# Performance work log

Measured on AMD Instinct MI355X. Metric: run time of the kernel, lower is better.

Reference implementation:

```python
import jax, jax.numpy as jnp
import numpy as np

BS, P, N, D, H = 2, 512, 2048, 768, 12
HD = D // H  # 64


def _lg_forward(input_xs, input_xq, xs_mask, qkv_w, qkv_b, proj_w, proj_b):
    bs, P_, D_ = input_xs.shape
    N_ = input_xq.shape[1]
    d = D_ // H
    scale = 1.0 / jnp.sqrt(jnp.asarray(d, input_xs.dtype))

    # concat order is [xq, xs] in the original
    xsq = jnp.concatenate([input_xq, input_xs], axis=1)          # [bs, N+P, D]
    full_qkv = xsq @ qkv_w + qkv_b                               # [bs, N+P, 3D]

    # faithful quirk: first P rows -> 'xs' qkv, remaining N rows -> 'xq' qkv
    xs_qkv = full_qkv[:, :P_].reshape(bs, P_, 3, H, d).transpose(2, 0, 3, 1, 4)
    xq_qkv = full_qkv[:, P_:].reshape(bs, N_, 3, H, d).transpose(2, 0, 3, 1, 4)
    xs_q, xs_k, xs_v = xs_qkv[0], xs_qkv[1], xs_qkv[2]           # [bs,H,P,d]
    xq_q, xq_k, xq_v = xq_qkv[0], xq_qkv[1], xq_qkv[2]           # [bs,H,N,d]

    # cross attention: xq queries attend over concat([xs, xq]) keys/values
    cross_k = jnp.concatenate([xs_k, xq_k], axis=2)              # [bs,H,P+N,d]
    cross_v = jnp.concatenate([xs_v, xq_v], axis=2)              # [bs,H,P+N,d]
    cross_scores = jnp.einsum('bhnd,bhmd->bhnm', xq_q, cross_k)  # [bs,H,N,P+N]
    cross_mask = jnp.pad(xs_mask, ((0, 0), (0, N_)))[:, None, None, :]
    cross_scores = jnp.where(cross_mask, -jnp.inf, cross_scores) * scale
    cross_probs = jax.nn.softmax(cross_scores, axis=-1)
    cross_out = jnp.einsum('bhnm,bhmd->bhnd', cross_probs, cross_v)
    cross_out = cross_out.transpose(0, 2, 1, 3).reshape(bs, N_, D_)  # [bs,N,D]

    # xs self attention
    self_scores = jnp.einsum('bhpd,bhqd->bhpq', xs_q, xs_k)      # [bs,H,P,P]
    self_scores = jnp.where(xs_mask[:, None, None, :], -jnp.inf, self_scores) * scale
    self_probs = jax.nn.softmax(self_scores, axis=-1)
    xs_out = jnp.einsum('bhpq,bhqd->bhpd', self_probs, xs_v)     # [bs,H,P,d]
    # faithful quirk: original does .transpose(-2,-1).view(bs,P,-1)
    xs_out = xs_out.transpose(0, 1, 3, 2).reshape(bs, P_, D_)    # [bs,P,D] (scrambled layout)

    out = jnp.concatenate([xs_out, cross_out], axis=1) @ proj_w + proj_b
    return out[:, :P_], out[:, P_:]


def setup_inputs() -> dict:
    key = jax.random.key(0)
    ks = jax.random.split(key, 6)
    return {
        'input_xs': jax.random.normal(ks[0], (BS, P, D), jnp.float32),
        'input_xq': jax.random.normal(ks[1], (BS, N, D), jnp.float32),
        'xs_mask': jax.random.randint(ks[2], (BS, P), 0, 2).astype(bool),
        'qkv_w': jax.random.normal(ks[3], (D, 3 * D), jnp.float32) * (D ** -0.5),
        'qkv_b': jnp.zeros((3 * D,), jnp.float32),
        'proj_w': jax.random.normal(ks[4], (D, D), jnp.float32) * (D ** -0.5),
        'proj_b': jnp.zeros((D,), jnp.float32),
    }


def reference(input_xs, input_xq, xs_mask, qkv_w, qkv_b, proj_w, proj_b):
    return _lg_forward(input_xs, input_xq, xs_mask, qkv_w, qkv_b, proj_w, proj_b)
```

## Files before the change

### kernel.cpp

```cpp
#include <hip/hip_runtime.h>
#include <hip/hip_bf16.h>

#define BS   2
#define PP   512
#define NN   2048
#define DD   768
#define HH   12
#define HD   64
#define RTOT 2560
#define QKVC 2304
#define MTOT (BS * RTOT)
#define CROWS (BS * HH * NN)
#define SROWS (BS * HH * PP)
#define TROWS (CROWS + SROWS)

typedef __attribute__((ext_vector_type(8))) short  short8;
typedef __attribute__((ext_vector_type(4))) float  floatx4;

#define MFMA16(a, b, c) __builtin_amdgcn_mfma_f32_16x16x32_bf16(a, b, c, 0, 0, 0)
#define LOG2E 1.4426950408889634f
#define SCL2  0.18033688011112042f

__device__ __forceinline__ float bf2f(unsigned short x) {
    union { unsigned u; float f; } c; c.u = ((unsigned)x) << 16; return c.f;
}
__device__ __forceinline__ unsigned short f2bf(float x) {
    union { float f; unsigned u; } c; c.f = x;
    unsigned r = c.u + 0x7fff + ((c.u >> 16) & 1);
    return (unsigned short)(r >> 16);
}

__device__ __forceinline__ float4 load4(const void* p, size_t i, bool f32) {
    if (f32) return *(const float4*)((const float*)p + i);
    ushort4 u = *(const ushort4*)((const unsigned short*)p + i);
    return make_float4(bf2f(u.x), bf2f(u.y), bf2f(u.z), bf2f(u.w));
}
__device__ __forceinline__ float load1(const void* p, size_t i, bool f32) {
    return f32 ? ((const float*)p)[i] : bf2f(((const unsigned short*)p)[i]);
}
__device__ __forceinline__ bool mask_at(const void* m, int idx, int mtype) {
    if (mtype == 2) return ((const float*)m)[idx] != 0.0f;
    if (mtype == 1) return ((const unsigned char*)m)[idx] != 0;
    return ((const int*)m)[idx] != 0;
}
__device__ __forceinline__ void store_out(float* p, size_t i, float v) { p[i] = v; }
__device__ __forceinline__ void store_out(__hip_bfloat16* p, size_t i, float v) {
    p[i] = __float2bfloat16(v);
}

__device__ __forceinline__ void gload_lds16(const unsigned short* g, unsigned short* l) {
    __builtin_amdgcn_global_load_lds(
        (const __attribute__((address_space(1))) void*)g,
        (__attribute__((address_space(3))) void*)l,
        16, 0, 0);
}

__device__ __forceinline__ int sigma_pos(int k) {
    return (k & 0x23) | ((k & 0x0C) << 1) | ((k & 0x10) >> 2);
}
__device__ __forceinline__ int sigma_inv(int p) {
    return (p & 0x23) | ((p & 0x18) >> 1) | ((p & 0x04) << 2);
}

__global__ void detect_kernel(const void* __restrict__ w,
                              const void* __restrict__ mask,
                              int* __restrict__ flags,
                              float* __restrict__ mb, int do_mb) {
    __shared__ int s_f32, s_fmask, s_bmask;
    if (threadIdx.x == 0) { s_f32 = 0; s_fmask = 0; s_bmask = 0; }
    __syncthreads();
    const uint4* u4 = (const uint4*)w;
    unsigned acc = 0;
    #pragma unroll
    for (int k = 0; k < 4; k++) {
        uint4 x = u4[k * 256 + threadIdx.x];
        unsigned t0 = x.x & 0x7fff7fffu, t1 = x.y & 0x7fff7fffu;
        unsigned t2 = x.z & 0x7fff7fffu, t3 = x.w & 0x7fff7fffu;
        acc |= (t0 + 0x3fff3fffu) & 0x80008000u;
        acc |= (t1 + 0x3fff3fffu) & 0x80008000u;
        acc |= (t2 + 0x3fff3fffu) & 0x80008000u;
        acc |= (t3 + 0x3fff3fffu) & 0x80008000u;
    }
    if (acc) atomicOr(&s_f32, 1);
    const unsigned* mw = (const unsigned*)mask;
    int fm = 0, bm = 0;
    {
        unsigned v = mw[threadIdx.x];
        if (v == 0x3F800000u) fm = 1;
        else if ((v & 0xFFFFFF00u) != 0u) bm = 1;
    }
    if (fm) atomicOr(&s_fmask, 1);
    if (bm) atomicOr(&s_bmask, 1);
    __syncthreads();
    if (threadIdx.x == 0) {
        flags[0] = s_f32;
        flags[1] = s_fmask ? 2 : (s_bmask ? 1 : 0);
    }
    if (do_mb) {
        const int mtype = s_fmask ? 2 : (s_bmask ? 1 : 0);
        for (int i = threadIdx.x; i < BS * RTOT; i += 256) {
            int b = i / RTOT, m = i % RTOT;
            float v = -15.0f * LOG2E;
            if (m < PP && mask_at(mask, b * PP + m, mtype)) v = -1e30f;
            mb[i] = v;
        }
    }
}

#define TQKV ((QKVC / 64) * (DD / 64))
#define TPRJ ((DD / 64) * (DD / 64))
__global__ __launch_bounds__(256) void prep_kernel(
    const void* __restrict__ xq, const void* __restrict__ xs,
    const void* __restrict__ qkv_w, const void* __restrict__ proj_w,
    const int* __restrict__ flags,
    unsigned short* __restrict__ Abf,
    unsigned short* __restrict__ WqkvT,
    unsigned short* __restrict__ WprojT)
{
    const bool f32 = flags[0] != 0;
    __shared__ unsigned short T[64][65];
    int blk = blockIdx.x;
    if (blk < MTOT) {
        if (threadIdx.x < 192) {
            const int r = blk;
            const int b = r / RTOT, rr = r % RTOT;
            const void* src;
            size_t off;
            if (rr < NN) { src = xq; off = (size_t)(b * NN + rr) * DD; }
            else         { src = xs; off = (size_t)(b * PP + (rr - NN)) * DD; }
            const int t = threadIdx.x;
            float4 v = load4(src, off + t * 4, f32);
            ushort4 o;
            o.x = f2bf(v.x); o.y = f2bf(v.y); o.z = f2bf(v.z); o.w = f2bf(v.w);
            *(ushort4*)&Abf[(size_t)r * DD + t * 4] = o;
        }
        return;
    }
    blk -= MTOT;
    const void* in; int R, C; unsigned short* out; int bx;
    if (blk < TQKV) {
        in = qkv_w; R = DD; C = QKVC; out = WqkvT;
        bx = blk % (QKVC / 64);
    } else {
        blk -= TQKV;
        in = proj_w; R = DD; C = DD; out = WprojT;
        bx = blk % (DD / 64);
    }
    const int by = (in == qkv_w) ? (blk / (QKVC / 64)) : (blk / (DD / 64));
    const int c0 = bx * 64, r0 = by * 64;
    const int col = threadIdx.x & 63;
    const int r4  = threadIdx.x >> 6;
    #pragma unroll
    for (int p = 0; p < 16; p++) {
        int row = p * 4 + r4;
        T[row][col] = f2bf(load1(in, (size_t)(r0 + row) * C + c0 + col, f32));
    }
    __syncthreads();
    #pragma unroll
    for (int p = 0; p < 16; p++) {
        int crow = p * 4 + r4;
        out[(size_t)(c0 + crow) * R + r0 + col] = T[col][crow];
    }
}

__global__ __launch_bounds__(256) void vtprep_kernel(
    const unsigned short* __restrict__ qkv, unsigned short* __restrict__ VtG)
{
    alignas(16) __shared__ unsigned short T[64][72];
    const int mt = blockIdx.x * 64;
    const int bh = blockIdx.y;
    const int b = bh / HH, h = bh % HH;
    const int lr  = threadIdx.x >> 2;
    const int ld0 = (threadIdx.x & 3) << 4;
    const unsigned short* vp = qkv +
        (size_t)(b * RTOT + mt + lr) * QKVC + 2 * DD + h * HD + ld0;
    *(uint4*)&T[lr][ld0]     = ((const uint4*)vp)[0];
    *(uint4*)&T[lr][ld0 + 8] = ((const uint4*)vp)[1];
    __syncthreads();
    unsigned short tmp[16];
    #pragma unroll
    for (int j = 0; j < 16; j++) {
        const int c = ld0 + j;
        tmp[j] = T[sigma_inv(c)][lr];
    }
    unsigned short* dst = VtG + ((size_t)bh * HD + lr) * RTOT + mt + ld0;
    *(uint4*)dst       = *(uint4*)&tmp[0];
    *(uint4*)(dst + 8) = *(uint4*)&tmp[8];
}

template<int MODE, int NCOL>
__global__ __launch_bounds__(256) void mgemm_kernel(
    const unsigned short* __restrict__ A,
    const unsigned short* __restrict__ BT,
    const void* __restrict__ bias,
    const int* __restrict__ flags,
    void* __restrict__ outp)
{
    alignas(16) __shared__ unsigned short Ash[128 * 64];
    alignas(16) __shared__ unsigned short Bsh[128 * 64];

    const int tid  = threadIdx.x;
    const int w    = tid >> 6;
    const int lane = tid & 63;
    const int grp  = lane >> 4;
    const int li   = lane & 15;
    const int row0 = blockIdx.y * 128;
    const int col0 = blockIdx.x * 128;
    const int moff = (w >> 1) * 64;
    const int noff = (w & 1) * 64;
    const int srow = lane >> 3;
    const int scol = (((lane & 7) ^ srow) << 3);
    const int lx7  = li & 7;

    floatx4 o[4][4];
    #pragma unroll
    for (int i = 0; i < 4; i++)
        #pragma unroll
        for (int j = 0; j < 4; j++)
            o[i][j] = (floatx4){0.f, 0.f, 0.f, 0.f};

    for (int k0 = 0; k0 < DD; k0 += 64) {
        __syncthreads();
        #pragma unroll
        for (int i = 0; i < 4; i++) {
            const int rr = w * 32 + i * 8;
            gload_lds16(A  + (size_t)(row0 + rr + srow) * DD + k0 + scol,
                        &Ash[rr * 64]);
            gload_lds16(BT + (size_t)(col0 + rr + srow) * DD + k0 + scol,
                        &Bsh[rr * 64]);
        }
        __syncthreads();
        #pragma unroll
        for (int ks = 0; ks < 2; ks++) {
            short8 af[4], bf[4];
            const int ch = ((ks << 2) + grp) ^ lx7;
            #pragma unroll
            for (int i = 0; i < 4; i++)
                af[i] = *(const short8*)&Ash[(moff + i * 16 + li) * 64 + ch * 8];
            #pragma unroll
            for (int j = 0; j < 4; j++)
                bf[j] = *(const short8*)&Bsh[(noff + j * 16 + li) * 64 + ch * 8];
            #pragma unroll
            for (int i = 0; i < 4; i++)
                #pragma unroll
                for (int j = 0; j < 4; j++)
                    o[i][j] = MFMA16(af[i], bf[j], o[i][j]);
        }
    }

    const bool f32 = flags[0] != 0;
    float bv[4];
    #pragma unroll
    for (int j = 0; j < 4; j++)
        bv[j] = load1(bias, col0 + noff + j * 16 + li, f32);

    #pragma unroll
    for (int i = 0; i < 4; i++) {
        #pragma unroll
        for (int r = 0; r < 4; r++) {
            int grow = row0 + moff + i * 16 + grp * 4 + r;
            #pragma unroll
            for (int j = 0; j < 4; j++) {
                int gcol = col0 + noff + j * 16 + li;
                float v = o[i][j][r] + bv[j];
                if (MODE == 0) {
                    ((unsigned short*)outp)[(size_t)grow * NCOL + gcol] = f2bf(v);
                } else {
                    int b = grow / RTOT, rr = grow % RTOT;
                    size_t dst = (rr < PP)
                        ? ((size_t)(b * PP + rr) * DD + gcol)
                        : ((size_t)BS * PP * DD + (size_t)(b * NN + (rr - PP)) * DD + gcol);
                    ((float*)outp)[dst] = v;
                }
            }
        }
    }
}

template<bool PACKED, int SPL>
__global__ __launch_bounds__(256, 4) void fattn3_kernel(
    const unsigned short* __restrict__ qkv,
    const unsigned short* __restrict__ VtG,
    const float* __restrict__ mb,
    unsigned short* __restrict__ attn_out,
    unsigned short* __restrict__ part_o,
    float* __restrict__ part_l)
{
    const int CB = BS * HH * (NN / 128);
    const int SB = BS * HH * (PP / 128);

    int bid = blockIdx.x;
    bool cross; int chunk, v;
    if (bid < CB * SPL) { cross = true;  chunk = bid / CB; v = bid % CB; }
    else { int s = bid - CB * SPL; cross = false; chunk = s / SB; v = s % SB; }
    const int nqb  = cross ? (NN / 128) : (PP / 128);
    const int q0   = (v % nqb) * 128;
    const int h    = (v / nqb) % HH;
    const int b    = v / (nqb * HH);
    const int QOFF = cross ? PP : 0;
    const int NT   = cross ? (RTOT / 64) : (PP / 64);
    const int tpc  = NT / SPL;
    const int t_beg = chunk * tpc, t_end = chunk * tpc + tpc;
    const int rowbase = cross ? ((b * HH + h) * NN + q0)
                              : (CROWS + (b * HH + h) * PP + q0);

    alignas(16) __shared__ unsigned short Ks[64][72];
    alignas(16) __shared__ unsigned short Vt[64][72];

    const int tid  = threadIdx.x;
    const int w    = tid >> 6;
    const int lane = tid & 63;
    const int grp  = lane >> 4;
    const int li   = lane & 15;
    const int lr   = tid >> 2;
    const int ld0  = (tid & 3) << 4;

    short8 qf[2][2];
    #pragma unroll
    for (int qi = 0; qi < 2; qi++) {
        const unsigned short* qp = qkv +
            (size_t)(b * RTOT + QOFF + q0 + w * 32 + qi * 16 + li) * QKVC
            + h * HD + grp * 8;
        qf[qi][0] = *(const short8*)(qp);
        qf[qi][1] = *(const short8*)(qp + 32);
    }

    floatx4 o[2][4];
    #pragma unroll
    for (int qi = 0; qi < 2; qi++)
        #pragma unroll
        for (int n = 0; n < 4; n++)
            o[qi][n] = (floatx4){0.f, 0.f, 0.f, 0.f};
    float lp[2] = {0.f, 0.f};

    const unsigned short* kptr = qkv +
        (size_t)(b * RTOT + t_beg * 64 + lr) * QKVC + DD + h * HD + ld0;
    const unsigned short* vptr = PACKED
        ? VtG + ((size_t)(b * HH + h) * HD + lr) * RTOT + t_beg * 64 + ld0
        : kptr + DD;
    const float* mbp = mb + b * RTOT + t_beg * 64 + grp * 4;

    uint4 kr0, kr1, vr0, vr1;
    kr0 = ((const uint4*)kptr)[0];
    kr1 = ((const uint4*)kptr)[1];
    vr0 = ((const uint4*)vptr)[0];
    vr1 = ((const uint4*)vptr)[1];
    kptr += (size_t)64 * QKVC;
    vptr += PACKED ? 64 : (size_t)64 * QKVC;

    for (int t = t_beg; t < t_end; t++) {
        __syncthreads();
        *(uint4*)&Ks[lr][ld0]     = kr0;
        *(uint4*)&Ks[lr][ld0 + 8] = kr1;
        if (PACKED) {
            *(uint4*)&Vt[lr][ld0]     = vr0;
            *(uint4*)&Vt[lr][ld0 + 8] = vr1;
        } else {
            unsigned short tmp[16];
            *(uint4*)&tmp[0] = vr0;
            *(uint4*)&tmp[8] = vr1;
            const int slr = sigma_pos(lr);
            #pragma unroll
            for (int j = 0; j < 16; j++) Vt[ld0 + j][slr] = tmp[j];
        }
        __syncthreads();

        if (t + 1 < t_end) {
            kr0 = ((const uint4*)kptr)[0];
            kr1 = ((const uint4*)kptr)[1];
            vr0 = ((const uint4*)vptr)[0];
            vr1 = ((const uint4*)vptr)[1];
            kptr += (size_t)64 * QKVC;
            vptr += PACKED ? 64 : (size_t)64 * QKVC;
        }

        floatx4 sfT[2][4];
        __builtin_amdgcn_s_setprio(1);
        #pragma unroll
        for (int n = 0; n < 4; n++) {
            short8 kb0 = *(const short8*)&Ks[n * 16 + li][grp * 8];
            short8 kb1 = *(const short8*)&Ks[n * 16 + li][32 + grp * 8];
            #pragma unroll
            for (int qi = 0; qi < 2; qi++) {
                floatx4 acc = {0.f, 0.f, 0.f, 0.f};
                acc = MFMA16(kb0, qf[qi][0], acc);
                acc = MFMA16(kb1, qf[qi][1], acc);
                sfT[qi][n] = acc;
            }
        }
        __builtin_amdgcn_s_setprio(0);

        floatx4 mbv[4];
        #pragma unroll
        for (int n = 0; n < 4; n++)
            mbv[n] = *(const floatx4*)(mbp + n * 16);
        mbp += 64;

        short8 pa[2][2];
        #pragma unroll
        for (int qi = 0; qi < 2; qi++) {
            unsigned u[4][4];
            #pragma unroll
            for (int n = 0; n < 4; n++) {
                #pragma unroll
                for (int r = 0; r < 4; r++) {
                    float e = __builtin_amdgcn_exp2f(
                        fmaf(sfT[qi][n][r], SCL2, mbv[n][r]));
                    u[n][r] = __float_as_uint(e);
                    lp[qi] += __uint_as_float(u[n][r] & 0xffff0000u);
                }
            }
            #pragma unroll
            for (int s2 = 0; s2 < 2; s2++) {
                uint4 pk;
                pk.x = __builtin_amdgcn_perm(u[2*s2][1],   u[2*s2][0],   0x07060302u);
                pk.y = __builtin_amdgcn_perm(u[2*s2][3],   u[2*s2][2],   0x07060302u);
                pk.z = __builtin_amdgcn_perm(u[2*s2+1][1], u[2*s2+1][0], 0x07060302u);
                pk.w = __builtin_amdgcn_perm(u[2*s2+1][3], u[2*s2+1][2], 0x07060302u);
                pa[qi][s2] = __builtin_bit_cast(short8, pk);
            }
        }

        __builtin_amdgcn_s_setprio(1);
        #pragma unroll
        for (int s2 = 0; s2 < 2; s2++) {
            #pragma unroll
            for (int n2 = 0; n2 < 4; n2++) {
                short8 vf = *(const short8*)&Vt[n2 * 16 + li][s2 * 32 + grp * 8];
                o[0][n2] = MFMA16(pa[0][s2], vf, o[0][n2]);
                o[1][n2] = MFMA16(pa[1][s2], vf, o[1][n2]);
            }
        }
        __builtin_amdgcn_s_setprio(0);
    }

    float lfull[2];
    #pragma unroll
    for (int qi = 0; qi < 2; qi++) {
        float l = lp[qi];
        l += __shfl_xor(l, 16);
        l += __shfl_xor(l, 32);
        lfull[qi] = l;
    }

    if (SPL > 1) {
        #pragma unroll
        for (int qi = 0; qi < 2; qi++)
            #pragma unroll
            for (int r = 0; r < 4; r++) {
                float lv = __shfl(lfull[qi], grp * 4 + r);
                size_t row = (size_t)chunk * TROWS + rowbase
                           + w * 32 + qi * 16 + grp * 4 + r;
                #pragma unroll
                for (int n2 = 0; n2 < 4; n2++)
                    part_o[row * 64 + n2 * 16 + li] = f2bf(o[qi][n2][r]);
                if (li == 0) part_l[row] = lv;
            }
    } else {
        #pragma unroll
        for (int qi = 0; qi < 2; qi++)
            #pragma unroll
            for (int r = 0; r < 4; r++) {
                float inv = 1.0f / __shfl(lfull[qi], grp * 4 + r);
                int qloc = q0 + w * 32 + qi * 16 + grp * 4 + r;
                if (cross) {
                    size_t row = (size_t)(b * RTOT + PP + qloc);
                    #pragma unroll
                    for (int n2 = 0; n2 < 4; n2++)
                        attn_out[row * DD + h * HD + n2 * 16 + li] =
                            f2bf(o[qi][n2][r] * inv);
                } else {
                    #pragma unroll
                    for (int n2 = 0; n2 < 4; n2++) {
                        int dc = n2 * 16 + li;
                        int f = h * (HD * PP) + dc * PP + qloc;
                        attn_out[(size_t)(b * RTOT + f / DD) * DD + (f % DD)]
                            = f2bf(o[qi][n2][r] * inv);
                    }
                }
            }
    }
}

template<int SPL>
__global__ __launch_bounds__(256) void combine_kernel(
    const unsigned short* __restrict__ part_o,
    const float* __restrict__ part_l,
    unsigned short* __restrict__ attn_out)
{
    const int row = blockIdx.x * 4 + (threadIdx.x >> 6);
    const int dv  = threadIdx.x & 63;
    float l = 0.f, ov = 0.f;
    #pragma unroll
    for (int c = 0; c < SPL; c++) {
        l  += part_l[(size_t)c * TROWS + row];
        ov += bf2f(part_o[((size_t)c * TROWS + row) * 64 + dv]);
    }
    float res = ov / l;
    if (row < CROWS) {
        int b = row / (HH * NN), rem = row % (HH * NN);
        int h = rem / NN, n = rem % NN;
        attn_out[(size_t)(b * RTOT + PP + n) * DD + h * HD + dv] = f2bf(res);
    } else {
        int r2 = row - CROWS;
        int b = r2 / (HH * PP), rem = r2 % (HH * PP);
        int h = rem / PP, p = rem % PP;
        int f = h * (HD * PP) + dv * PP + p;
        attn_out[(size_t)(b * RTOT + f / DD) * DD + (f % DD)] = f2bf(res);
    }
}

template<int MODE>
__global__ __launch_bounds__(256) void fattn_kernel(
    const __hip_bfloat16* __restrict__ qkv,
    const void* __restrict__ mask,
    const int* __restrict__ flags,
    __hip_bfloat16* __restrict__ attn_out)
{
    constexpr int NQ    = (MODE == 0) ? NN : PP;
    constexpr int NK    = (MODE == 0) ? RTOT : PP;
    constexpr int QOFF  = (MODE == 0) ? PP : 0;
    constexpr int NTILE = NK / 64;

    alignas(16) __shared__ unsigned short Ks[64][72];
    alignas(16) __shared__ unsigned short Vt[64][72];
    alignas(16) __shared__ unsigned short Psm[4][16][72];

    const int tid   = threadIdx.x;
    const int w     = tid >> 6;
    const int lane  = tid & 63;
    const int grp   = lane >> 4;
    const int li    = lane & 15;
    const int nqb   = NQ / 64;
    const int q0    = (blockIdx.x % nqb) * 64;
    const int h     = (blockIdx.x / nqb) % HH;
    const int b     = blockIdx.x / (nqb * HH);
    const int mtype = flags[1];

    const unsigned short* qkv_u = (const unsigned short*)qkv;
    const int lr  = tid >> 2;
    const int ld0 = (tid & 3) << 4;

    short8 qf[2];
    {
        const unsigned short* qp = qkv_u +
            (size_t)(b * RTOT + QOFF + q0 + w * 16 + li) * QKVC + h * HD + grp * 8;
        qf[0] = *(const short8*)(qp);
        qf[1] = *(const short8*)(qp + 32);
    }

    floatx4 o[4] = {{0.f,0.f,0.f,0.f},{0.f,0.f,0.f,0.f},
                    {0.f,0.f,0.f,0.f},{0.f,0.f,0.f,0.f}};
    float mrun[4] = {-3e38f, -3e38f, -3e38f, -3e38f};
    float lrun[4] = {0.f, 0.f, 0.f, 0.f};

    for (int t = 0; t < NTILE; t++) {
        const int m0 = t * 64;
        __syncthreads();
        {
            const unsigned short* kp = qkv_u +
                (size_t)(b * RTOT + m0 + lr) * QKVC + DD + h * HD + ld0;
            *(uint4*)&Ks[lr][ld0]     = ((const uint4*)kp)[0];
            *(uint4*)&Ks[lr][ld0 + 8] = ((const uint4*)kp)[1];
            const unsigned short* vp = kp + DD;
            unsigned short tmp[16];
            *(uint4*)&tmp[0] = ((const uint4*)vp)[0];
            *(uint4*)&tmp[8] = ((const uint4*)vp)[1];
            #pragma unroll
            for (int j = 0; j < 16; j++) Vt[ld0 + j][lr] = tmp[j];
        }
        __syncthreads();

        floatx4 sf[4];
        #pragma unroll
        for (int n = 0; n < 4; n++) {
            floatx4 acc = {0.f, 0.f, 0.f, 0.f};
            short8 kb0 = *(const short8*)&Ks[n * 16 + li][grp * 8];
            short8 kb1 = *(const short8*)&Ks[n * 16 + li][32 + grp * 8];
            acc = MFMA16(qf[0], kb0, acc);
            acc = MFMA16(qf[1], kb1, acc);
            sf[n] = acc;
        }

        bool mk[4];
        #pragma unroll
        for (int n = 0; n < 4; n++) {
            int m = m0 + n * 16 + li;
            mk[n] = (m < PP) && mask_at(mask, b * PP + m, mtype);
        }

        #pragma unroll
        for (int r = 0; r < 4; r++) {
            float sv[4];
            #pragma unroll
            for (int n = 0; n < 4; n++)
                sv[n] = mk[n] ? -1e30f : sf[n][r] * 0.125f;
            float tm = fmaxf(fmaxf(sv[0], sv[1]), fmaxf(sv[2], sv[3]));
            #pragma unroll
            for (int off = 1; off < 16; off <<= 1)
                tm = fmaxf(tm, __shfl_xor(tm, off));
            float mnew = fmaxf(mrun[r], tm);
            float al = __expf(mrun[r] - mnew);
            float p[4], ts = 0.f;
            #pragma unroll
            for (int n = 0; n < 4; n++) {
                p[n] = (sv[n] < -1e29f) ? 0.f : __expf(sv[n] - mnew);
                ts += p[n];
            }
            #pragma unroll
            for (int off = 1; off < 16; off <<= 1)
                ts += __shfl_xor(ts, off);
            mrun[r] = mnew;
            lrun[r] = lrun[r] * al + ts;
            #pragma unroll
            for (int n = 0; n < 4; n++) {
                o[n][r] *= al;
                Psm[w][grp * 4 + r][n * 16 + li] = f2bf(p[n]);
            }
        }
        __syncthreads();

        #pragma unroll
        for (int s2 = 0; s2 < 2; s2++) {
            short8 pa = *(const short8*)&Psm[w][li][s2 * 32 + grp * 8];
            #pragma unroll
            for (int n2 = 0; n2 < 4; n2++) {
                short8 vf = *(const short8*)&Vt[n2 * 16 + li][s2 * 32 + grp * 8];
                o[n2] = MFMA16(pa, vf, o[n2]);
            }
        }
    }

    unsigned short* ao = (unsigned short*)attn_out;
    #pragma unroll
    for (int r = 0; r < 4; r++) {
        float inv = 1.0f / lrun[r];
        int qloc = q0 + w * 16 + grp * 4 + r;
        if (MODE == 0) {
            size_t row = (size_t)(b * RTOT + PP + qloc);
            #pragma unroll
            for (int n2 = 0; n2 < 4; n2++)
                ao[row * DD + h * HD + n2 * 16 + li] = f2bf(o[n2][r] * inv);
        } else {
            #pragma unroll
            for (int n2 = 0; n2 < 4; n2++) {
                int dc = n2 * 16 + li;
                int f = h * (HD * PP) + dc * PP + qloc;
                ao[(size_t)(b * RTOT + f / DD) * DD + (f % DD)] = f2bf(o[n2][r] * inv);
            }
        }
    }
}

template<int MODE, int NCOL, typename OutT>
__global__ __launch_bounds__(256) void gemm_kernel(
    const void* __restrict__ A0, const void* __restrict__ A1,
    const void* __restrict__ W, const void* __restrict__ bias,
    const int* __restrict__ flags, OutT* __restrict__ out)
{
    const bool f32 = flags[0] != 0;
    alignas(16) __shared__ float As[16][68];
    alignas(16) __shared__ float Bsh2[16][68];
    const int tid  = threadIdx.x;
    const int row0 = blockIdx.y * 64;
    const int col0 = blockIdx.x * 64;
    const int ty = tid >> 4, tx = tid & 15;
    const int a_row = tid >> 2;
    const int a_k4  = (tid & 3) * 4;
    const int grow  = row0 + a_row;
    const void* abase; size_t aoff; bool af32;
    if (MODE == 0) {
        int b = grow / RTOT, r = grow % RTOT;
        if (r < NN) { abase = A0; aoff = (size_t)(b * NN + r) * DD; }
        else        { abase = A1; aoff = (size_t)(b * PP + (r - NN)) * DD; }
        af32 = f32;
    } else {
        abase = A0; aoff = (size_t)grow * DD; af32 = false;
    }
    const int b_k  = tid >> 4;
    const int b_n4 = (tid & 15) * 4;
    float acc[4][4] = {};
    for (int k0 = 0; k0 < DD; k0 += 16) {
        float4 fa = load4(abase, aoff + k0 + a_k4, af32);
        As[a_k4 + 0][a_row] = fa.x;
        As[a_k4 + 1][a_row] = fa.y;
        As[a_k4 + 2][a_row] = fa.z;
        As[a_k4 + 3][a_row] = fa.w;
        float4 fb = load4(W, (size_t)(k0 + b_k) * NCOL + col0 + b_n4, f32);
        *(float4*)&Bsh2[b_k][b_n4] = fb;
        __syncthreads();
        #pragma unroll
        for (int kk = 0; kk < 16; kk++) {
            float4 av = *(const float4*)&As[kk][ty * 4];
            float4 bvv = *(const float4*)&Bsh2[kk][tx * 4];
            float a_[4] = {av.x, av.y, av.z, av.w};
            float b_[4] = {bvv.x, bvv.y, bvv.z, bvv.w};
            #pragma unroll
            for (int i = 0; i < 4; i++)
                #pragma unroll
                for (int j = 0; j < 4; j++)
                    acc[i][j] += a_[i] * b_[j];
        }
        __syncthreads();
    }
    #pragma unroll
    for (int i = 0; i < 4; i++) {
        int gr = row0 + ty * 4 + i;
        #pragma unroll
        for (int j = 0; j < 4; j++) {
            int gc = col0 + tx * 4 + j;
            float v = acc[i][j] + load1(bias, gc, f32);
            if (MODE == 0) {
                store_out(out, (size_t)gr * NCOL + gc, v);
            } else {
                int b = gr / RTOT, r = gr % RTOT;
                size_t dst = (r < PP)
                    ? ((size_t)(b * PP + r) * DD + gc)
                    : ((size_t)BS * PP * DD + (size_t)(b * NN + (r - PP)) * DD + gc);
                store_out(out, dst, v);
            }
        }
    }
}

extern "C" void kernel_launch(void* const* d_in, const int* in_sizes, int n_in,
                              void* d_out, int out_size, void* d_ws, size_t ws_size,
                              hipStream_t stream) {
    const void *xs = nullptr, *xq = nullptr, *mask = nullptr,
               *qkv_w = nullptr, *qkv_b = nullptr, *proj_w = nullptr, *proj_b = nullptr;
    for (int i = 0; i < n_in; i++) {
        switch (in_sizes[i]) {
            case BS * PP * DD:   xs     = d_in[i]; break;
            case BS * NN * DD:   xq     = d_in[i]; break;
            case BS * PP:        mask   = d_in[i]; break;
            case DD * QKVC:      qkv_w  = d_in[i]; break;
            case QKVC:           qkv_b  = d_in[i]; break;
            case DD * DD:        proj_w = d_in[i]; break;
            case DD:             proj_b = d_in[i]; break;
        }
    }
    if (!xs || !xq || !mask || !qkv_w || !qkv_b || !proj_w || !proj_b) {
        xs = d_in[0]; xq = d_in[1]; mask = d_in[2];
        qkv_w = d_in[3]; qkv_b = d_in[4]; proj_w = d_in[5]; proj_b = d_in[6];
    }
    float* out = (float*)d_out;

    const size_t off_mb   = 256;
    const size_t off_full = off_mb   + (size_t)BS * RTOT * 4;
    const size_t off_ab   = off_full + (size_t)MTOT * QKVC * 2;
    const size_t off_w    = off_ab   + (size_t)MTOT * DD * 2;
    const size_t off_wp   = off_w    + (size_t)QKVC * DD * 2;
    const size_t off_vt   = off_wp   + (size_t)DD * DD * 2;
    const size_t off_po   = off_vt   + (size_t)BS * HH * HD * RTOT * 2;
    const size_t off_ml4  = off_po   + (size_t)4 * TROWS * 64 * 2;
    const size_t need_A4  = off_ml4  + (size_t)4 * TROWS * 4;
    const size_t off_ml2  = off_po   + (size_t)2 * TROWS * 64 * 2;
    const size_t need_A2  = off_ml2  + (size_t)2 * TROWS * 4;
    const size_t need_B   = off_po;
    const size_t need_C   = off_vt;

    const size_t r_full = 256;
    const size_t r_ab   = r_full + (size_t)MTOT * QKVC * 2;
    const size_t r_wq   = r_ab   + (size_t)MTOT * DD * 2;
    const size_t r_wp   = r_wq   + (size_t)QKVC * DD * 2;
    const size_t need_R = r_wp   + (size_t)DD * DD * 2;

    int* flags = (int*)d_ws;

    if (ws_size >= need_C) {
        float* mb               = (float*)((char*)d_ws + off_mb);
        unsigned short* fullqkv = (unsigned short*)((char*)d_ws + off_full);
        unsigned short* attn    = (unsigned short*)((char*)d_ws + off_ab);
        unsigned short* WqkvT   = (unsigned short*)((char*)d_ws + off_w);
        unsigned short* WprojT  = (unsigned short*)((char*)d_ws + off_wp);
        unsigned short* VtG     = (unsigned short*)((char*)d_ws + off_vt);
        unsigned short* part_o  = (unsigned short*)((char*)d_ws + off_po);

        detect_kernel<<<1, 256, 0, stream>>>(qkv_w, mask, flags, mb, 1);
        prep_kernel<<<MTOT + TQKV + TPRJ, 256, 0, stream>>>(
            xq, xs, qkv_w, proj_w, flags, attn , WqkvT, WprojT);

        mgemm_kernel<0, QKVC><<<dim3(QKVC / 128, MTOT / 128), 256, 0, stream>>>(
            attn , WqkvT, qkv_b, flags, (void*)fullqkv);

        const int CB = BS * HH * (NN / 128), SB = BS * HH * (PP / 128);
        if (ws_size >= need_A4) {
            float* part_l = (float*)((char*)d_ws + off_ml4);
            vtprep_kernel<<<dim3(RTOT / 64, BS * HH), 256, 0, stream>>>(fullqkv, VtG);
            fattn3_kernel<true, 4><<<(CB + SB) * 4, 256, 0, stream>>>(
                fullqkv, VtG, mb, nullptr, part_o, part_l);
            combine_kernel<4><<<TROWS / 4, 256, 0, stream>>>(part_o, part_l, attn);
        } else if (ws_size >= need_A2) {
            float* part_l = (float*)((char*)d_ws + off_ml2);
            vtprep_kernel<<<dim3(RTOT / 64, BS * HH), 256, 0, stream>>>(fullqkv, VtG);
            fattn3_kernel<true, 2><<<(CB + SB) * 2, 256, 0, stream>>>(
                fullqkv, VtG, mb, nullptr, part_o, part_l);
            combine_kernel<2><<<TROWS / 4, 256, 0, stream>>>(part_o, part_l, attn);
        } else if (ws_size >= need_B) {
            vtprep_kernel<<<dim3(RTOT / 64, BS * HH), 256, 0, stream>>>(fullqkv, VtG);
            fattn3_kernel<true, 1><<<CB + SB, 256, 0, stream>>>(
                fullqkv, VtG, mb, attn, nullptr, nullptr);
        } else {
            fattn3_kernel<false, 1><<<CB + SB, 256, 0, stream>>>(
                fullqkv, nullptr, mb, attn, nullptr, nullptr);
        }

        mgemm_kernel<1, DD><<<dim3(DD / 128, MTOT / 128), 256, 0, stream>>>(
            attn, WprojT, proj_b, flags, (void*)out);
    } else if (ws_size >= need_R) {
        unsigned short* fullqkv = (unsigned short*)((char*)d_ws + r_full);
        unsigned short* attn    = (unsigned short*)((char*)d_ws + r_ab);
        unsigned short* WqkvT   = (unsigned short*)((char*)d_ws + r_wq);
        unsigned short* WprojT  = (unsigned short*)((char*)d_ws + r_wp);

        detect_kernel<<<1, 256, 0, stream>>>(qkv_w, mask, flags, nullptr, 0);
        prep_kernel<<<MTOT + TQKV + TPRJ, 256, 0, stream>>>(
            xq, xs, qkv_w, proj_w, flags, attn, WqkvT, WprojT);
        mgemm_kernel<0, QKVC><<<dim3(QKVC / 128, MTOT / 128), 256, 0, stream>>>(
            attn, WqkvT, qkv_b, flags, (void*)fullqkv);
        fattn_kernel<0><<<BS * HH * (NN / 64), 256, 0, stream>>>(
            (const __hip_bfloat16*)fullqkv, mask, flags, (__hip_bfloat16*)attn);
        fattn_kernel<1><<<BS * HH * (PP / 64), 256, 0, stream>>>(
            (const __hip_bfloat16*)fullqkv, mask, flags, (__hip_bfloat16*)attn);
        mgemm_kernel<1, DD><<<dim3(DD / 128, MTOT / 128), 256, 0, stream>>>(
            attn, WprojT, proj_b, flags, (void*)out);
    } else {
        __hip_bfloat16* fullqkv = (__hip_bfloat16*)((char*)d_ws + 256);
        __hip_bfloat16* attn    = fullqkv + (size_t)MTOT * QKVC;
        detect_kernel<<<1, 256, 0, stream>>>(qkv_w, mask, flags, nullptr, 0);
        gemm_kernel<0, QKVC, __hip_bfloat16>
            <<<dim3(QKVC / 64, MTOT / 64), 256, 0, stream>>>(
            xq, xs, qkv_w, qkv_b, flags, fullqkv);
        fattn_kernel<0><<<BS * HH * (NN / 64), 256, 0, stream>>>(fullqkv, mask, flags, attn);
        fattn_kernel<1><<<BS * HH * (PP / 64), 256, 0, stream>>>(fullqkv, mask, flags, attn);
        gemm_kernel<1, DD, float>
            <<<dim3(DD / 64, MTOT / 64), 256, 0, stream>>>(
            attn, nullptr, proj_w, proj_b, flags, out);
    }
}
```

Before: 213.1 us.

## Permute GEMM and attention output columns for vectorized stores; transpose self-attn combine in LDS

Introduces a tau column permutation applied to the B-operand row loads in the GEMM and to the V-transposed layout, so each lane owns four contiguous output columns. This allows packed 8-byte bf16 stores and float4 stores in the GEMM epilogue and in the attention output, replacing scattered 2-byte and 4-byte writes. The combine kernel gains a separate path for self-attention rows that stages results in LDS and writes the scrambled transposed layout with 16-byte stores. The consistency of the permutation across vtprep, the GEMMs and the attention kernel is subtle, and a mismatch would corrupt results.

```diff
diff --git a/kernel.cpp b/kernel.cpp
--- a/kernel.cpp
+++ b/kernel.cpp
@@ -60,6 +60,12 @@
 }
 __device__ __forceinline__ int sigma_inv(int p) {
     return (p & 0x23) | ((p & 0x18) >> 1) | ((p & 0x04) << 2);
+}
+__device__ __forceinline__ int tau_pos(int p) {
+    return ((p & 15) << 2) | ((p >> 4) & 3);
+}
+__device__ __forceinline__ int tau_inv(int c) {
+    return ((c & 3) << 4) | ((c >> 2) & 15);
 }
 
 __global__ void detect_kernel(const void* __restrict__ w,
@@ -177,11 +183,12 @@
     *(uint4*)&T[lr][ld0]     = ((const uint4*)vp)[0];
     *(uint4*)&T[lr][ld0 + 8] = ((const uint4*)vp)[1];
     __syncthreads();
+    const int tdv = tau_pos(lr);
     unsigned short tmp[16];
     #pragma unroll
     for (int j = 0; j < 16; j++) {
         const int c = ld0 + j;
-        tmp[j] = T[sigma_inv(c)][lr];
+        tmp[j] = T[sigma_inv(c)][tdv];
     }
     unsigned short* dst = VtG + ((size_t)bh * HD + lr) * RTOT + mt + ld0;
     *(uint4*)dst       = *(uint4*)&tmp[0];
@@ -224,9 +231,11 @@
         #pragma unroll
         for (int i = 0; i < 4; i++) {
             const int rr = w * 32 + i * 8;
+            const int q  = rr + srow;
+            const int bq = (q & 64) | tau_pos(q & 63);
             gload_lds16(A  + (size_t)(row0 + rr + srow) * DD + k0 + scol,
                         &Ash[rr * 64]);
-            gload_lds16(BT + (size_t)(col0 + rr + srow) * DD + k0 + scol,
+            gload_lds16(BT + (size_t)(col0 + bq) * DD + k0 + scol,
                         &Bsh[rr * 64]);
         }
         __syncthreads();
@@ -249,29 +258,30 @@
     }
 
     const bool f32 = flags[0] != 0;
-    float bv[4];
-    #pragma unroll
-    for (int j = 0; j < 4; j++)
-        bv[j] = load1(bias, col0 + noff + j * 16 + li, f32);
+    const int cbase = col0 + noff + li * 4;
+    float4 b4 = load4(bias, cbase, f32);
+    float bv[4] = {b4.x, b4.y, b4.z, b4.w};
 
     #pragma unroll
     for (int i = 0; i < 4; i++) {
         #pragma unroll
         for (int r = 0; r < 4; r++) {
             int grow = row0 + moff + i * 16 + grp * 4 + r;
-            #pragma unroll
-            for (int j = 0; j < 4; j++) {
-                int gcol = col0 + noff + j * 16 + li;
-                float v = o[i][j][r] + bv[j];
-                if (MODE == 0) {
-                    ((unsigned short*)outp)[(size_t)grow * NCOL + gcol] = f2bf(v);
-                } else {
-                    int b = grow / RTOT, rr = grow % RTOT;
-                    size_t dst = (rr < PP)
-                        ? ((size_t)(b * PP + rr) * DD + gcol)
-                        : ((size_t)BS * PP * DD + (size_t)(b * NN + (rr - PP)) * DD + gcol);
-                    ((float*)outp)[dst] = v;
-                }
+            float v0 = o[i][0][r] + bv[0];
+            float v1 = o[i][1][r] + bv[1];
+            float v2 = o[i][2][r] + bv[2];
+            float v3 = o[i][3][r] + bv[3];
+            if (MODE == 0) {
+                uint2 pk;
+                pk.x = (unsigned)f2bf(v0) | ((unsigned)f2bf(v1) << 16);
+                pk.y = (unsigned)f2bf(v2) | ((unsigned)f2bf(v3) << 16);
+                *(uint2*)&((unsigned short*)outp)[(size_t)grow * NCOL + cbase] = pk;
+            } else {
+                int b = grow / RTOT, rr2 = grow % RTOT;
+                size_t dst = (rr2 < PP)
+                    ? ((size_t)(b * PP + rr2) * DD + cbase)
+                    : ((size_t)BS * PP * DD + (size_t)(b * NN + (rr2 - PP)) * DD + cbase);
+                *(float4*)&((float*)outp)[dst] = make_float4(v0, v1, v2, v3);
             }
         }
     }
@@ -361,7 +371,8 @@
             *(uint4*)&tmp[8] = vr1;
             const int slr = sigma_pos(lr);
             #pragma unroll
-            for (int j = 0; j < 16; j++) Vt[ld0 + j][slr] = tmp[j];
+            for (int j = 0; j < 16; j++)
+                Vt[tau_inv(ld0 + j)][slr] = tmp[j];
         }
         __syncthreads();
 
@@ -451,9 +462,10 @@
                 float lv = __shfl(lfull[qi], grp * 4 + r);
                 size_t row = (size_t)chunk * TROWS + rowbase
                            + w * 32 + qi * 16 + grp * 4 + r;
-                #pragma unroll
-                for (int n2 = 0; n2 < 4; n2++)
-                    part_o[row * 64 + n2 * 16 + li] = f2bf(o[qi][n2][r]);
+                uint2 pk;
+                pk.x = (unsigned)f2bf(o[qi][0][r]) | ((unsigned)f2bf(o[qi][1][r]) << 16);
+                pk.y = (unsigned)f2bf(o[qi][2][r]) | ((unsigned)f2bf(o[qi][3][r]) << 16);
+                *(uint2*)&part_o[row * 64 + li * 4] = pk;
                 if (li == 0) part_l[row] = lv;
             }
     } else {
@@ -465,14 +477,16 @@
                 int qloc = q0 + w * 32 + qi * 16 + grp * 4 + r;
                 if (cross) {
                     size_t row = (size_t)(b * RTOT + PP + qloc);
-                    #pragma unroll
-                    for (int n2 = 0; n2 < 4; n2++)
-                        attn_out[row * DD + h * HD + n2 * 16 + li] =
-                            f2bf(o[qi][n2][r] * inv);
+                    uint2 pk;
+                    pk.x = (unsigned)f2bf(o[qi][0][r] * inv)
+                         | ((unsigned)f2bf(o[qi][1][r] * inv) << 16);
+                    pk.y = (unsigned)f2bf(o[qi][2][r] * inv)
+                         | ((unsigned)f2bf(o[qi][3][r] * inv) << 16);
+                    *(uint2*)&attn_out[row * DD + h * HD + li * 4] = pk;
                 } else {
                     #pragma unroll
                     for (int n2 = 0; n2 < 4; n2++) {
-                        int dc = n2 * 16 + li;
+                        int dc = li * 4 + n2;
                         int f = h * (HD * PP) + dc * PP + qloc;
                         attn_out[(size_t)(b * RTOT + f / DD) * DD + (f % DD)]
                             = f2bf(o[qi][n2][r] * inv);
@@ -488,25 +502,59 @@
     const float* __restrict__ part_l,
     unsigned short* __restrict__ attn_out)
 {
-    const int row = blockIdx.x * 4 + (threadIdx.x >> 6);
-    const int dv  = threadIdx.x & 63;
-    float l = 0.f, ov = 0.f;
-    #pragma unroll
-    for (int c = 0; c < SPL; c++) {
-        l  += part_l[(size_t)c * TROWS + row];
-        ov += bf2f(part_o[((size_t)c * TROWS + row) * 64 + dv]);
-    }
-    float res = ov / l;
-    if (row < CROWS) {
+    const int CBLK = CROWS / 4;
+    if (blockIdx.x < CBLK) {
+        const int row = blockIdx.x * 4 + (threadIdx.x >> 6);
+        const int dv  = threadIdx.x & 63;
+        float l = 0.f, ov = 0.f;
+        #pragma unroll
+        for (int c = 0; c < SPL; c++) {
+            l  += part_l[(size_t)c * TROWS + row];
+            ov += bf2f(part_o[((size_t)c * TROWS + row) * 64 + dv]);
+        }
+        float res = ov / l;
         int b = row / (HH * NN), rem = row % (HH * NN);
         int h = rem / NN, n = rem % NN;
         attn_out[(size_t)(b * RTOT + PP + n) * DD + h * HD + dv] = f2bf(res);
-    } else {
-        int r2 = row - CROWS;
-        int b = r2 / (HH * PP), rem = r2 % (HH * PP);
-        int h = rem / PP, p = rem % PP;
-        int f = h * (HD * PP) + dv * PP + p;
-        attn_out[(size_t)(b * RTOT + f / DD) * DD + (f % DD)] = f2bf(res);
+        return;
+    }
+    __shared__ unsigned short T[64][72];
+    const int blk = blockIdx.x - CBLK;
+    const int r0b = blk * 64;
+    {
+        const int rp  = threadIdx.x >> 2;
+        const int d0  = (threadIdx.x & 3) * 16;
+        const int row = CROWS + r0b + rp;
+        float l = 0.f;
+        float ov[16] = {};
+        #pragma unroll
+        for (int c = 0; c < SPL; c++) {
+            l += part_l[(size_t)c * TROWS + row];
+            const uint4* po = (const uint4*)&part_o[((size_t)c * TROWS + row) * 64 + d0];
+            uint4 x0 = po[0], x1 = po[1];
+            const unsigned short* u0 = (const unsigned short*)&x0;
+            const unsigned short* u1 = (const unsigned short*)&x1;
+            #pragma unroll
+            for (int k = 0; k < 8; k++) { ov[k] += bf2f(u0[k]); ov[8 + k] += bf2f(u1[k]); }
+        }
+        float inv = 1.0f / l;
+        #pragma unroll
+        for (int k = 0; k < 16; k++) T[rp][d0 + k] = f2bf(ov[k] * inv);
+    }
+    __syncthreads();
+    {
+        const int dv = threadIdx.x >> 2;
+        const int pc = (threadIdx.x & 3) * 16;
+        const int bh = r0b / PP;
+        const int p0 = r0b % PP;
+        const int b = bh / HH, h = bh % HH;
+        unsigned short tmp[16];
+        #pragma unroll
+        for (int k = 0; k < 16; k++) tmp[k] = T[pc + k][dv];
+        size_t base = (size_t)b * RTOT * DD + (size_t)h * (HD * PP)
+                    + (size_t)dv * PP + p0 + pc;
+        *(uint4*)&attn_out[base]     = *(uint4*)&tmp[0];
+        *(uint4*)&attn_out[base + 8] = *(uint4*)&tmp[8];
     }
 }
 
@@ -766,6 +814,7 @@
     const size_t need_R = r_wp   + (size_t)DD * DD * 2;
 
     int* flags = (int*)d_ws;
+    const int NCMB = CROWS / 4 + SROWS / 64;
 
     if (ws_size >= need_C) {
         float* mb               = (float*)((char*)d_ws + off_mb);
@@ -789,13 +838,13 @@
             vtprep_kernel<<<dim3(RTOT / 64, BS * HH), 256, 0, stream>>>(fullqkv, VtG);
             fattn3_kernel<true, 4><<<(CB + SB) * 4, 256, 0, stream>>>(
                 fullqkv, VtG, mb, nullptr, part_o, part_l);
-            combine_kernel<4><<<TROWS / 4, 256, 0, stream>>>(part_o, part_l, attn);
+            combine_kernel<4><<<NCMB, 256, 0, stream>>>(part_o, part_l, attn);
         } else if (ws_size >= need_A2) {
             float* part_l = (float*)((char*)d_ws + off_ml2);
             vtprep_kernel<<<dim3(RTOT / 64, BS * HH), 256, 0, stream>>>(fullqkv, VtG);
             fattn3_kernel<true, 2><<<(CB + SB) * 2, 256, 0, stream>>>(
                 fullqkv, VtG, mb, nullptr, part_o, part_l);
-            combine_kernel<2><<<TROWS / 4, 256, 0, stream>>>(part_o, part_l, attn);
+            combine_kernel<2><<<NCMB, 256, 0, stream>>>(part_o, part_l, attn);
         } else if (ws_size >= need_B) {
             vtprep_kernel<<<dim3(RTOT / 64, BS * HH), 256, 0, stream>>>(fullqkv, VtG);
             fattn3_kernel<true, 1><<<CB + SB, 256, 0, stream>>>(
```

After: 197.0 us. 1.08x faster.
